# Kernel tuning notes

Measured on AMD Instinct MI355X. Metric: run time of the kernel, lower is better.

Reference implementation:

```python
import jax, jax.numpy as jnp
import numpy as np

N, IN_F, OUT_F = 1024, 256, 1024

def setup_inputs() -> dict:
    key = jax.random.key(0)
    k1, k2 = jax.random.split(key)
    x = jax.random.normal(k1, (N, IN_F), dtype=jnp.float32)
    centres = jax.random.normal(k2, (OUT_F, IN_F), dtype=jnp.float32)  # normal_(0,1) init
    log_sigmas = jnp.zeros((OUT_F,), dtype=jnp.float32)  # constant_(0) init
    return {"x": x, "centres": centres, "log_sigmas": log_sigmas}

def reference(x, centres, log_sigmas):
    # diff: (N, out_features, in_features) broadcast, matching torch expand
    diff = x[:, None, :] - centres[None, :, :]
    # Euclidean distance then per-centre sigma scaling: (N, out_features)
    distances = jnp.sqrt(jnp.sum(diff * diff, axis=-1)) / jnp.exp(log_sigmas)[None, :]
    # gaussian basis function: exp(-0.5 * d^2)
    return jnp.exp(-0.5 * distances * distances)
```

## Files before the change

### kernel.cpp

```cpp
#include <hip/hip_runtime.h>
#include <math.h>

#define K_FEAT 256
#define M_OUT  1024
#define N_ROWS 1024

#define TM 32
#define TN 32
#define LSTR 264

typedef short bf16x8 __attribute__((ext_vector_type(8)));
typedef float f32x4  __attribute__((ext_vector_type(4)));

__global__ __launch_bounds__(256) void row_norms(
    const float* __restrict__ x, const float* __restrict__ c,
    float* __restrict__ norms)
{
    const int lane = threadIdx.x & 63;
    const int wave = threadIdx.x >> 6;
    const int row  = blockIdx.x * 4 + wave;
    const float* src = (row < N_ROWS) ? (x + (size_t)row * K_FEAT)
                                      : (c + (size_t)(row - N_ROWS) * K_FEAT);
    const float4 v = ((const float4*)src)[lane];
    float s = v.x * v.x + v.y * v.y + v.z * v.z + v.w * v.w;
    #pragma unroll
    for (int off = 32; off; off >>= 1) s += __shfl_down(s, off, 64);
    if (lane == 0) norms[row] = s;
}

__global__ __launch_bounds__(256, 4) void rbf_mfma(
    const float* __restrict__ x,
    const float* __restrict__ centres,
    const float* __restrict__ log_sigmas,
    const float* __restrict__ norms,
    float* __restrict__ out)
{
    __shared__ unsigned short xs[TM * LSTR];
    __shared__ unsigned short cs[TN * LSTR];

    const int tid  = threadIdx.x;
    const int lane = tid & 63;
    const int wave = tid >> 6;
    const int row_base = blockIdx.y * TM;
    const int col_base = blockIdx.x * TN;

    #pragma unroll
    for (int l = 0; l < 8; ++l) {
        const int  li    = l & 3;
        const int  chunk = tid + li * 256;
        const int  row   = chunk >> 5;
        const int  k0    = (chunk & 31) * 8;
        const float* src = (l < 4)
            ? (x       + (size_t)(row_base + row) * K_FEAT + k0)
            : (centres + (size_t)(col_base + row) * K_FEAT + k0);
        const float4 v0 = ((const float4*)src)[0];
        const float4 v1 = ((const float4*)src)[1];
        uint4 p;
        p.x = (__float_as_uint(v0.x) >> 16) | (__float_as_uint(v0.y) & 0xffff0000u);
        p.y = (__float_as_uint(v0.z) >> 16) | (__float_as_uint(v0.w) & 0xffff0000u);
        p.z = (__float_as_uint(v1.x) >> 16) | (__float_as_uint(v1.y) & 0xffff0000u);
        p.w = (__float_as_uint(v1.z) >> 16) | (__float_as_uint(v1.w) & 0xffff0000u);
        unsigned short* dst = (l < 4) ? &xs[row * LSTR + k0] : &cs[row * LSTR + k0];
        *(uint4*)dst = p;
    }
    __syncthreads();

    const int m    = lane & 15;
    const int quad = lane >> 4;
    const int tr   = (wave & 1) * 16;
    const int tc   = (wave >> 1) * 16;
    f32x4 acc = {0.f, 0.f, 0.f, 0.f};
    const unsigned short* ap = &xs[(tr + m) * LSTR + quad * 8];
    const unsigned short* bp = &cs[(tc + m) * LSTR + quad * 8];
    #pragma unroll
    for (int kk = 0; kk < 8; ++kk) {
        const bf16x8 a = *(const bf16x8*)(ap + kk * 32);
        const bf16x8 b = *(const bf16x8*)(bp + kk * 32);
        acc = __builtin_amdgcn_mfma_f32_16x16x32_bf16(a, b, acc, 0, 0, 0);
    }

    const int   col = col_base + tc + m;
    const float i2s = __expf(-2.0f * log_sigmas[col]);
    const float ncv = norms[N_ROWS + col];
    #pragma unroll
    for (int i = 0; i < 4; ++i) {
        const int   r   = tr + quad * 4 + i;
        const float nxv = norms[row_base + r];
        const float d2  = nxv + ncv - 2.0f * acc[i];
        out[(size_t)(row_base + r) * M_OUT + col] = __expf(-0.5f * d2 * i2s);
    }
}

extern "C" void kernel_launch(void* const* d_in, const int* in_sizes, int n_in,
                              void* d_out, int out_size, void* d_ws, size_t ws_size,
                              hipStream_t stream) {
    const float* x  = (const float*)d_in[0];
    const float* c  = (const float*)d_in[1];
    const float* ls = (const float*)d_in[2];
    float* out   = (float*)d_out;
    float* norms = (float*)d_ws;

    row_norms<<<dim3(2 * N_ROWS / 4), dim3(256), 0, stream>>>(x, c, norms);
    dim3 grid(M_OUT / TN, N_ROWS / TM);
    rbf_mfma<<<grid, dim3(256), 0, stream>>>(x, c, ls, norms, out);
}
```

Measured before the change: 63.17 us.

## Pre-convert inputs to bf16 in prep kernel and enlarge row tile

The norm kernel becomes a prep kernel that also writes bf16 copies of x and centres into the workspace, halved norms, and per-centre scale factors. The main kernel then loads bf16 directly, halving global reads per tile and skipping repeated fp32-to-bf16 conversion. The row tile doubles to 64 so each wave computes two MFMA tiles sharing one A fragment, and the epilogue is folded algebraically into a single multiply and exp. This trades an extra workspace write for fewer redundant loads and fewer blocks, with launch bounds lowered to 2 blocks per CU.

```diff
diff --git a/kernel.cpp b/kernel.cpp
--- a/kernel.cpp
+++ b/kernel.cpp
@@ -5,38 +5,63 @@
 #define M_OUT  1024
 #define N_ROWS 1024
 
-#define TM 32
+#define TM 64
 #define TN 32
 #define LSTR 264
 
 typedef short bf16x8 __attribute__((ext_vector_type(8)));
 typedef float f32x4  __attribute__((ext_vector_type(4)));
 
-__global__ __launch_bounds__(256) void row_norms(
+#define WS_CB_OFF   (N_ROWS * K_FEAT)
+#define WS_F32_OFF  (2 * N_ROWS * K_FEAT * 2)
+
+__global__ __launch_bounds__(256) void prep(
     const float* __restrict__ x, const float* __restrict__ c,
-    float* __restrict__ norms)
+    const float* __restrict__ ls, void* __restrict__ ws)
 {
     const int lane = threadIdx.x & 63;
     const int wave = threadIdx.x >> 6;
     const int row  = blockIdx.x * 4 + wave;
-    const float* src = (row < N_ROWS) ? (x + (size_t)row * K_FEAT)
-                                      : (c + (size_t)(row - N_ROWS) * K_FEAT);
+    unsigned short* bf = (unsigned short*)ws;
+    float* hnx = (float*)((char*)ws + WS_F32_OFF);
+    float* hnc = hnx + N_ROWS;
+    float* sc  = hnc + M_OUT;
+
+    const bool is_x = row < N_ROWS;
+    const float* src = is_x ? (x + (size_t)row * K_FEAT)
+                            : (c + (size_t)(row - N_ROWS) * K_FEAT);
     const float4 v = ((const float4*)src)[lane];
+    uint2 p;
+    p.x = (__float_as_uint(v.x) >> 16) | (__float_as_uint(v.y) & 0xffff0000u);
+    p.y = (__float_as_uint(v.z) >> 16) | (__float_as_uint(v.w) & 0xffff0000u);
+    unsigned short* dst = bf + (is_x ? (size_t)row * K_FEAT
+                                     : (size_t)WS_CB_OFF + (size_t)(row - N_ROWS) * K_FEAT);
+    *(uint2*)(dst + lane * 4) = p;
+
     float s = v.x * v.x + v.y * v.y + v.z * v.z + v.w * v.w;
     #pragma unroll
     for (int off = 32; off; off >>= 1) s += __shfl_down(s, off, 64);
-    if (lane == 0) norms[row] = s;
+    if (lane == 0) {
+        if (is_x) hnx[row] = 0.5f * s;
+        else {
+            const int m = row - N_ROWS;
+            hnc[m] = 0.5f * s;
+            sc[m]  = __expf(-2.0f * ls[m]);
+        }
+    }
 }
 
-__global__ __launch_bounds__(256, 4) void rbf_mfma(
-    const float* __restrict__ x,
-    const float* __restrict__ centres,
-    const float* __restrict__ log_sigmas,
-    const float* __restrict__ norms,
-    float* __restrict__ out)
+__global__ __launch_bounds__(256, 2) void rbf_mfma(
+    const void* __restrict__ ws, float* __restrict__ out)
 {
     __shared__ unsigned short xs[TM * LSTR];
     __shared__ unsigned short cs[TN * LSTR];
+
+    const unsigned short* xb = (const unsigned short*)ws;
+    const unsigned short* cb = xb + WS_CB_OFF;
+    const float* hnx = (const float*)((const char*)ws + WS_F32_OFF);
+    const float* hnc = hnx + N_ROWS;
+    const float* sc  = hnc + M_OUT;
 
     const int tid  = threadIdx.x;
     const int lane = tid & 63;
@@ -45,49 +70,47 @@
     const int col_base = blockIdx.x * TN;
 
     #pragma unroll
-    for (int l = 0; l < 8; ++l) {
-        const int  li    = l & 3;
-        const int  chunk = tid + li * 256;
-        const int  row   = chunk >> 5;
-        const int  k0    = (chunk & 31) * 8;
-        const float* src = (l < 4)
-            ? (x       + (size_t)(row_base + row) * K_FEAT + k0)
-            : (centres + (size_t)(col_base + row) * K_FEAT + k0);
-        const float4 v0 = ((const float4*)src)[0];
-        const float4 v1 = ((const float4*)src)[1];
-        uint4 p;
-        p.x = (__float_as_uint(v0.x) >> 16) | (__float_as_uint(v0.y) & 0xffff0000u);
-        p.y = (__float_as_uint(v0.z) >> 16) | (__float_as_uint(v0.w) & 0xffff0000u);
-        p.z = (__float_as_uint(v1.x) >> 16) | (__float_as_uint(v1.y) & 0xffff0000u);
-        p.w = (__float_as_uint(v1.z) >> 16) | (__float_as_uint(v1.w) & 0xffff0000u);
-        unsigned short* dst = (l < 4) ? &xs[row * LSTR + k0] : &cs[row * LSTR + k0];
-        *(uint4*)dst = p;
+    for (int l = 0; l < 12; ++l) {
+        const int chunk = tid + l * 256;
+        const int row   = chunk >> 5;
+        const int k0    = (chunk & 31) * 8;
+        const unsigned short* src = (l < 8)
+            ? (xb + (size_t)(row_base + row) * K_FEAT + k0)
+            : (cb + (size_t)(col_base + row - TM) * K_FEAT + k0);
+        unsigned short* dst = (l < 8) ? &xs[row * LSTR + k0]
+                                      : &cs[(row - TM) * LSTR + k0];
+        *(uint4*)dst = *(const uint4*)src;
     }
     __syncthreads();
 
     const int m    = lane & 15;
     const int quad = lane >> 4;
-    const int tr   = (wave & 1) * 16;
-    const int tc   = (wave >> 1) * 16;
-    f32x4 acc = {0.f, 0.f, 0.f, 0.f};
-    const unsigned short* ap = &xs[(tr + m) * LSTR + quad * 8];
-    const unsigned short* bp = &cs[(tc + m) * LSTR + quad * 8];
+    const int slab = wave * 16;
+    f32x4 acc0 = {0.f, 0.f, 0.f, 0.f};
+    f32x4 acc1 = {0.f, 0.f, 0.f, 0.f};
+    const unsigned short* ap  = &xs[(slab + m) * LSTR + quad * 8];
+    const unsigned short* bp0 = &cs[ m       * LSTR + quad * 8];
+    const unsigned short* bp1 = &cs[(16 + m) * LSTR + quad * 8];
     #pragma unroll
     for (int kk = 0; kk < 8; ++kk) {
-        const bf16x8 a = *(const bf16x8*)(ap + kk * 32);
-        const bf16x8 b = *(const bf16x8*)(bp + kk * 32);
-        acc = __builtin_amdgcn_mfma_f32_16x16x32_bf16(a, b, acc, 0, 0, 0);
+        const bf16x8 a  = *(const bf16x8*)(ap  + kk * 32);
+        const bf16x8 b0 = *(const bf16x8*)(bp0 + kk * 32);
+        const bf16x8 b1 = *(const bf16x8*)(bp1 + kk * 32);
+        acc0 = __builtin_amdgcn_mfma_f32_16x16x32_bf16(a, b0, acc0, 0, 0, 0);
+        acc1 = __builtin_amdgcn_mfma_f32_16x16x32_bf16(a, b1, acc1, 0, 0, 0);
     }
 
-    const int   col = col_base + tc + m;
-    const float i2s = __expf(-2.0f * log_sigmas[col]);
-    const float ncv = norms[N_ROWS + col];
+    const int   col0 = col_base + m;
+    const int   col1 = col_base + 16 + m;
+    const float s0 = sc[col0],  s1 = sc[col1];
+    const float h0 = hnc[col0], h1 = hnc[col1];
     #pragma unroll
     for (int i = 0; i < 4; ++i) {
-        const int   r   = tr + quad * 4 + i;
-        const float nxv = norms[row_base + r];
-        const float d2  = nxv + ncv - 2.0f * acc[i];
-        out[(size_t)(row_base + r) * M_OUT + col] = __expf(-0.5f * d2 * i2s);
+        const int   r   = slab + quad * 4 + i;
+        const float hx  = hnx[row_base + r];
+        float* o = out + (size_t)(row_base + r) * M_OUT;
+        o[col0] = __expf((acc0[i] - hx - h0) * s0);
+        o[col1] = __expf((acc1[i] - hx - h1) * s1);
     }
 }
 
@@ -97,10 +120,9 @@
     const float* x  = (const float*)d_in[0];
     const float* c  = (const float*)d_in[1];
     const float* ls = (const float*)d_in[2];
-    float* out   = (float*)d_out;
-    float* norms = (float*)d_ws;
+    float* out = (float*)d_out;
 
-    row_norms<<<dim3(2 * N_ROWS / 4), dim3(256), 0, stream>>>(x, c, norms);
+    prep<<<dim3(2 * N_ROWS / 4), dim3(256), 0, stream>>>(x, c, ls, d_ws);
     dim3 grid(M_OUT / TN, N_ROWS / TM);
-    rbf_mfma<<<grid, dim3(256), 0, stream>>>(x, c, ls, norms, out);
+    rbf_mfma<<<grid, dim3(256), 0, stream>>>(d_ws, out);
 }
```

After: 62.47 us. No clear change (-1.1%).
